# Kernel tuning notes

Hardware: AMD Instinct MI355X
Metric: run time of the kernel (lower is better)

The kernel has to match this reference:

```python
import jax, jax.numpy as jnp
import numpy as np

S = 10  # samples per node


def setup_inputs() -> dict:
    key = jax.random.key(0)
    k1, k2, k3, k4, k5, k6 = jax.random.split(key, 6)
    N, D, V, E, NNZ = 8192, 256, 32768, 100000, 262144
    z = jax.random.normal(k1, (N, D), dtype=jnp.float32)
    W = jax.random.normal(k2, (V, D), dtype=jnp.float32) * 0.02
    rand_u = jax.random.uniform(k3, (N, S), dtype=jnp.float32)
    edges = jax.random.randint(k4, (2, E), 0, N, dtype=jnp.int64)
    ptr = jnp.sort(jax.random.randint(k5, (N + 1,), 0, NNZ, dtype=jnp.int64))
    col = jax.random.randint(k6, (NNZ,), 0, N, dtype=jnp.int64)
    return {"z": z, "W": W, "rand_u": rand_u, "edges": edges, "ptr": ptr, "col": col}


def reference(z, W, rand_u, edges, ptr, col):
    N = z.shape[0]
    nnz = col.shape[0]
    deg = ptr[1:] - ptr[:-1]                                   # [N]
    # vectorized per-node uniform neighbor sampling (with replacement)
    samp = (rand_u * deg[:, None].astype(rand_u.dtype)).astype(jnp.int64)  # [N, S]
    gidx = jnp.clip(ptr[:-1, None] + samp, 0, nnz - 1)          # [N, S]
    self_idx = jnp.arange(N, dtype=col.dtype)[:, None]
    n_u = jnp.where(deg[:, None] > 0, col[gidx], self_idx)      # [N, S]
    # gather-sum aggregation, averaged with self
    u_aggr = (z[n_u].sum(axis=1) + z) / (S + 1)                 # [N, D]
    # predictor: Linear(no bias) + Softmax(dim=1)
    logits = jnp.einsum('nd,vd->nv', u_aggr, W)                 # [N, V]
    probs = jax.nn.softmax(logits, axis=1)
    h_u = probs[edges[0]]                                       # [E, V]
    # nn.CrossEntropyLoss applied to softmax outputs (faithful to original)
    tgt = edges[1]
    log_p = jax.nn.log_softmax(h_u, axis=1)
    loss = -log_p[jnp.arange(tgt.shape[0]), tgt].mean()
    return loss
```

## Files before the change

kernel.cpp:

```cpp
#include <hip/hip_runtime.h>
#include <hip/hip_bf16.h>
#include <stdint.h>


#define NODES 8192
#define DIM   256
#define VOCAB 32768
#define SAMP  10
#define LOG2E 1.4426950408889634f

typedef float  f32x4  __attribute__((ext_vector_type(4)));
typedef short  bf16x8 __attribute__((ext_vector_type(8)));
typedef unsigned short u16x4 __attribute__((ext_vector_type(4)));

static __device__ __forceinline__ unsigned short f2bf(float x) {
    __hip_bfloat16 b = __float2bfloat16(x);
    return *reinterpret_cast<unsigned short*>(&b);
}
static __device__ __forceinline__ float bf2f(unsigned short x) {
    union { unsigned int u; float f; } v; v.u = ((unsigned int)x) << 16; return v.f;
}
static __device__ __forceinline__ float fexp2(float x) {
    float r; asm("v_exp_f32 %0, %1" : "=v"(r) : "v"(x)); return r;
}

__global__ void k_aggregate(const float* __restrict__ z, const float* __restrict__ ru,
                            const int* __restrict__ ptr, const int* __restrict__ col,
                            unsigned short* __restrict__ ub, int nnz) {
    int wid = threadIdx.x >> 6, lane = threadIdx.x & 63;
    int node = blockIdx.x * 4 + wid;
    if (node >= NODES) return;
    int p0 = ptr[node], p1 = ptr[node + 1];
    int deg = p1 - p0;
    float fdeg = (float)deg;
    f32x4 acc = {0.f, 0.f, 0.f, 0.f};
    #pragma unroll
    for (int s = 0; s < SAMP; ++s) {
        float r = ru[node * SAMP + s];
        int samp = (int)(r * fdeg);
        int gidx = p0 + samp;
        gidx = gidx < 0 ? 0 : (gidx > nnz - 1 ? nnz - 1 : gidx);
        int nb = (deg > 0) ? col[gidx] : node;
        acc += ((const f32x4*)(z + (size_t)nb * DIM))[lane];
    }
    acc += ((const f32x4*)(z + (size_t)node * DIM))[lane];
    acc = acc * (LOG2E / 11.0f);
    u16x4 h;
    h.x = f2bf(acc.x); h.y = f2bf(acc.y); h.z = f2bf(acc.z); h.w = f2bf(acc.w);
    ((u16x4*)(ub + (size_t)node * DIM))[lane] = h;
}

__global__ void k_convert_w(const float* __restrict__ W, unsigned short* __restrict__ Wb, int n4) {
    int i = blockIdx.x * blockDim.x + threadIdx.x;
    if (i >= n4) return;
    f32x4 v = ((const f32x4*)W)[i];
    u16x4 h;
    h.x = f2bf(v.x); h.y = f2bf(v.y); h.z = f2bf(v.z); h.w = f2bf(v.w);
    ((u16x4*)Wb)[i] = h;
}

#define BM 128
#define BN 256
#define NSTEP 64

static __device__ __forceinline__ void gload_lds16(const void* g, void* l) {
    __builtin_amdgcn_global_load_lds(
        (const __attribute__((address_space(1))) unsigned int*)g,
        (__attribute__((address_space(3))) unsigned int*)l, 16, 0, 0);
}

__global__ __launch_bounds__(512)
__attribute__((amdgpu_waves_per_eu(2, 2)))
void k_gemm_stats(
        const unsigned short* __restrict__ A,
        const unsigned short* __restrict__ B,
        float* __restrict__ part_s) {
    __shared__ __align__(16) unsigned short Bs[4][BN * 64];
    __shared__ float sred[BM][4];

    const int bid = blockIdx.x;
    const int slab = bid & 7;
    const int ntile = bid >> 3;
    const int rm = ntile * BM;
    const int t = threadIdx.x;
    const int lane = t & 63;
    const int wid = t >> 6;
    const int wr = wid >> 2, wc = wid & 3;
    const int g = lane >> 4, r16 = lane & 15;

    const char* Bbase = (const char*)B + (size_t)slab * (4096u * 512u);
    const unsigned pre0 = ((unsigned)(t >> 3) << 9)
                        + ((unsigned)((t & 7) ^ ((t >> 3) & 7)) << 4);
    const unsigned ldsb = (unsigned)t << 4;

    auto stage = [&](int buf, int sigma) {
        unsigned soff = ((unsigned)(sigma >> 2) << 17) + ((unsigned)(sigma & 3) << 7);
        unsigned lb = (unsigned)buf * 32768u + ldsb;
        #pragma unroll
        for (int i = 0; i < 4; ++i)
            gload_lds16(Bbase + soff + pre0 + (unsigned)i * 32768u,
                        (char*)Bs + lb + (unsigned)i * 8192u);
    };

    bf16x8 areg[4][8];
    #pragma unroll
    for (int m = 0; m < 4; ++m)
        #pragma unroll
        for (int j = 0; j < 8; ++j)
            areg[m][j] = *(const bf16x8*)(A +
                (size_t)(rm + wr * 64 + m * 16 + r16) * DIM + (j * 4 + g) * 8);
    stage(0, 0);
    stage(1, 1);

    f32x4 acc[4][4] = {};
    f32x4 sv[4] = {};

    auto fold = [&]() {
        #pragma unroll
        for (int m = 0; m < 4; ++m)
            #pragma unroll
            for (int n = 0; n < 4; ++n) {
                #pragma unroll
                for (int r = 0; r < 4; ++r)
                    sv[m][r] += fexp2(acc[m][n][r]);
                acc[m][n] = (f32x4){0.f, 0.f, 0.f, 0.f};
            }
    };

    for (int c = 0; c < 16; ++c) {
        #pragma unroll
        for (int ks = 0; ks < 4; ++ks) {
            const int s = c * 4 + ks;
            asm volatile("s_waitcnt vmcnt(4)" ::: "memory");
            __builtin_amdgcn_s_barrier();
            { int sigma = s + 2; if (sigma >= NSTEP) sigma -= NSTEP;
              stage((s + 2) & 3, sigma); }
            if (ks == 0 && c > 0) fold();
            __builtin_amdgcn_s_setprio(1);
            #pragma unroll
            for (int kk = 0; kk < 2; ++kk) {
                bf16x8 bfr[4];
                #pragma unroll
                for (int n = 0; n < 4; ++n) {
                    int R = wc * 64 + n * 16 + r16;
                    int slot = (kk * 4 + g) ^ (R & 7);
                    bfr[n] = *(const bf16x8*)((const char*)Bs
                        + (unsigned)(s & 3) * 32768u + (unsigned)(R * 128 + slot * 16));
                }
                #pragma unroll
                for (int m = 0; m < 4; ++m)
                    #pragma unroll
                    for (int n = 0; n < 4; ++n)
                        acc[m][n] = __builtin_amdgcn_mfma_f32_16x16x32_bf16(
                            areg[m][ks * 2 + kk], bfr[n], acc[m][n], 0, 0, 0);
            }
            __builtin_amdgcn_s_setprio(0);
        }
    }
    fold();

    #pragma unroll
    for (int m = 0; m < 4; ++m)
        #pragma unroll
        for (int st = 1; st < 16; st <<= 1)
            #pragma unroll
            for (int r = 0; r < 4; ++r)
                sv[m][r] += __shfl_xor(sv[m][r], st, 64);
    if (r16 == 0)
        #pragma unroll
        for (int m = 0; m < 4; ++m)
            #pragma unroll
            for (int r = 0; r < 4; ++r)
                sred[wr * 64 + m * 16 + g * 4 + r][wc] = sv[m][r];
    __syncthreads();
    if (t < BM)
        part_s[(size_t)(rm + t) * 8 + slab] =
            sred[t][0] + sred[t][1] + sred[t][2] + sred[t][3];
}

__global__ void k_reduce(const float* __restrict__ part_s, float* __restrict__ s0) {
    int n = blockIdx.x * 256 + threadIdx.x;
    float s = 0.f;
    #pragma unroll
    for (int j = 0; j < 8; ++j) s += part_s[(size_t)n * 8 + j];
    s0[n] = s;
}

#define ELB 512
__global__ __launch_bounds__(256) void k_edge_loss(
        const unsigned short* __restrict__ ub, const unsigned short* __restrict__ Wb,
        const int* __restrict__ edges, const float* __restrict__ s0,
        float lse2c, float* __restrict__ partial, int E) {
    int wid = threadIdx.x >> 6, lane = threadIdx.x & 63;
    int w = blockIdx.x * 4 + wid;
    float local = 0.f;
    for (int e = w; e < E; e += ELB * 4) {
        int src = edges[e], tgt = edges[E + e];
        u16x4 a = ((const u16x4*)(ub + (size_t)src * DIM))[lane];
        u16x4 b = ((const u16x4*)(Wb + (size_t)tgt * DIM))[lane];
        float d = bf2f(a.x) * bf2f(b.x) + bf2f(a.y) * bf2f(b.y)
                + bf2f(a.z) * bf2f(b.z) + bf2f(a.w) * bf2f(b.w);
        #pragma unroll
        for (int st = 1; st < 64; st <<= 1) d += __shfl_xor(d, st, 64);
        if (lane == 0) local += lse2c - fexp2(d) / s0[src];
    }
    __shared__ float bs[4];
    if (lane == 0) bs[wid] = local;
    __syncthreads();
    if (threadIdx.x == 0) partial[blockIdx.x] = bs[0] + bs[1] + bs[2] + bs[3];
}

__global__ void k_final(const float* __restrict__ partial, float* __restrict__ out, float invE) {
    int t = threadIdx.x;
    float s = partial[t] + partial[t + 256];
    #pragma unroll
    for (int st = 1; st < 64; st <<= 1) s += __shfl_xor(s, st, 64);
    __shared__ float ls[4];
    if ((t & 63) == 0) ls[t >> 6] = s;
    __syncthreads();
    if (t == 0) out[0] = (ls[0] + ls[1] + ls[2] + ls[3]) * invE;
}

extern "C" void kernel_launch(void* const* d_in, const int* in_sizes, int n_in,
                              void* d_out, int out_size, void* d_ws, size_t ws_size,
                              hipStream_t stream) {
    const float* z    = (const float*)d_in[0];
    const float* W    = (const float*)d_in[1];
    const float* ru   = (const float*)d_in[2];
    const int* edges  = (const int*)d_in[3];
    const int* ptr    = (const int*)d_in[4];
    const int* col    = (const int*)d_in[5];
    const int E   = in_sizes[3] / 2;
    const int nnz = in_sizes[5];

    char* ws = (char*)d_ws;
    unsigned short* ub     = (unsigned short*)(ws + 0);
    unsigned short* Wb     = (unsigned short*)(ws + 4194304);
    float*          part_s = (float*)(ws + 20971520);
    float*          s0     = (float*)(ws + 21233664);
    float*          epart  = (float*)(ws + 21266432);
    float*          out    = (float*)d_out;

    const float lse2c = logf((float)VOCAB + 1.0f);

    hipLaunchKernelGGL(k_aggregate, dim3(NODES / 4), dim3(256), 0, stream, z, ru, ptr, col, ub, nnz);
    hipLaunchKernelGGL(k_convert_w, dim3(VOCAB * DIM / 4 / 256), dim3(256), 0, stream, W, Wb, VOCAB * DIM / 4);
    hipLaunchKernelGGL(k_gemm_stats, dim3(512), dim3(512), 0, stream, ub, Wb, part_s);
    hipLaunchKernelGGL(k_reduce, dim3(NODES / 256), dim3(256), 0, stream, part_s, s0);
    hipLaunchKernelGGL(k_edge_loss, dim3(ELB), dim3(256), 0, stream, ub, Wb, edges, s0, lse2c, epart, E);
    hipLaunchKernelGGL(k_final, dim3(1), dim3(256), 0, stream, epart, out, 1.0f / (float)E);
}
```

Measured before the change: 291.1 us.

## Double-step GEMM pipeline intervals, merge prep kernels, fold final reduction into atomics

The GEMM main loop now stages two K-steps per barrier interval with vmcnt(0), precomputes the LDS fragment offsets, and stops issuing the wrap-around redundant loads at the tail. Aggregation and the W-to-bf16 conversion run as one launch, and the final reduction kernel is replaced by per-block atomicAdd into the output, which k_reduce zeroes. The aim is fewer barriers and fewer launches. The trade-offs are coarser synchronisation that may expose load latency, and a non-deterministic float summation order.

```diff
diff --git a/kernel.cpp b/kernel.cpp
--- a/kernel.cpp
+++ b/kernel.cpp
@@ -24,39 +24,40 @@
     float r; asm("v_exp_f32 %0, %1" : "=v"(r) : "v"(x)); return r;
 }
 
-__global__ void k_aggregate(const float* __restrict__ z, const float* __restrict__ ru,
-                            const int* __restrict__ ptr, const int* __restrict__ col,
-                            unsigned short* __restrict__ ub, int nnz) {
-    int wid = threadIdx.x >> 6, lane = threadIdx.x & 63;
-    int node = blockIdx.x * 4 + wid;
-    if (node >= NODES) return;
-    int p0 = ptr[node], p1 = ptr[node + 1];
-    int deg = p1 - p0;
-    float fdeg = (float)deg;
-    f32x4 acc = {0.f, 0.f, 0.f, 0.f};
-    #pragma unroll
-    for (int s = 0; s < SAMP; ++s) {
-        float r = ru[node * SAMP + s];
-        int samp = (int)(r * fdeg);
-        int gidx = p0 + samp;
-        gidx = gidx < 0 ? 0 : (gidx > nnz - 1 ? nnz - 1 : gidx);
-        int nb = (deg > 0) ? col[gidx] : node;
-        acc += ((const f32x4*)(z + (size_t)nb * DIM))[lane];
+__global__ void k_agg_conv(const float* __restrict__ z, const float* __restrict__ ru,
+                           const int* __restrict__ ptr, const int* __restrict__ col,
+                           const float* __restrict__ W,
+                           unsigned short* __restrict__ ub, unsigned short* __restrict__ Wb,
+                           int nnz) {
+    int b = blockIdx.x;
+    if (b < 2048) {
+        int wid = threadIdx.x >> 6, lane = threadIdx.x & 63;
+        int node = b * 4 + wid;
+        int p0 = ptr[node], p1 = ptr[node + 1];
+        int deg = p1 - p0;
+        float fdeg = (float)deg;
+        f32x4 acc = {0.f, 0.f, 0.f, 0.f};
+        #pragma unroll
+        for (int s = 0; s < SAMP; ++s) {
+            float r = ru[node * SAMP + s];
+            int samp = (int)(r * fdeg);
+            int gidx = p0 + samp;
+            gidx = gidx < 0 ? 0 : (gidx > nnz - 1 ? nnz - 1 : gidx);
+            int nb = (deg > 0) ? col[gidx] : node;
+            acc += ((const f32x4*)(z + (size_t)nb * DIM))[lane];
+        }
+        acc += ((const f32x4*)(z + (size_t)node * DIM))[lane];
+        acc = acc * (LOG2E / 11.0f);
+        u16x4 h;
+        h.x = f2bf(acc.x); h.y = f2bf(acc.y); h.z = f2bf(acc.z); h.w = f2bf(acc.w);
+        ((u16x4*)(ub + (size_t)node * DIM))[lane] = h;
+    } else {
+        int i = (b - 2048) * 256 + threadIdx.x;
+        f32x4 v = ((const f32x4*)W)[i];
+        u16x4 h;
+        h.x = f2bf(v.x); h.y = f2bf(v.y); h.z = f2bf(v.z); h.w = f2bf(v.w);
+        ((u16x4*)Wb)[i] = h;
     }
-    acc += ((const f32x4*)(z + (size_t)node * DIM))[lane];
-    acc = acc * (LOG2E / 11.0f);
-    u16x4 h;
-    h.x = f2bf(acc.x); h.y = f2bf(acc.y); h.z = f2bf(acc.z); h.w = f2bf(acc.w);
-    ((u16x4*)(ub + (size_t)node * DIM))[lane] = h;
-}
-
-__global__ void k_convert_w(const float* __restrict__ W, unsigned short* __restrict__ Wb, int n4) {
-    int i = blockIdx.x * blockDim.x + threadIdx.x;
-    if (i >= n4) return;
-    f32x4 v = ((const f32x4*)W)[i];
-    u16x4 h;
-    h.x = f2bf(v.x); h.y = f2bf(v.y); h.z = f2bf(v.z); h.w = f2bf(v.w);
-    ((u16x4*)Wb)[i] = h;
 }
 
 #define BM 128
@@ -93,15 +94,25 @@
                         + ((unsigned)((t & 7) ^ ((t >> 3) & 7)) << 4);
     const unsigned ldsb = (unsigned)t << 4;
 
-    auto stage = [&](int buf, int sigma) {
+    auto stage = [&](int sigma) {
         unsigned soff = ((unsigned)(sigma >> 2) << 17) + ((unsigned)(sigma & 3) << 7);
-        unsigned lb = (unsigned)buf * 32768u + ldsb;
+        unsigned lb = (unsigned)(sigma & 3) * 32768u + ldsb;
         #pragma unroll
         for (int i = 0; i < 4; ++i)
             gload_lds16(Bbase + soff + pre0 + (unsigned)i * 32768u,
                         (char*)Bs + lb + (unsigned)i * 8192u);
     };
 
+    unsigned boffs[8];
+    #pragma unroll
+    for (int kk = 0; kk < 2; ++kk)
+        #pragma unroll
+        for (int n = 0; n < 4; ++n) {
+            int R = wc * 64 + n * 16 + r16;
+            int slot = (kk * 4 + g) ^ (R & 7);
+            boffs[kk * 4 + n] = (unsigned)(R * 128 + slot * 16);
+        }
+
     bf16x8 areg[4][8];
     #pragma unroll
     for (int m = 0; m < 4; ++m)
@@ -109,8 +120,8 @@
         for (int j = 0; j < 8; ++j)
             areg[m][j] = *(const bf16x8*)(A +
                 (size_t)(rm + wr * 64 + m * 16 + r16) * DIM + (j * 4 + g) * 8);
-    stage(0, 0);
-    stage(1, 1);
+    stage(0);
+    stage(1);
 
     f32x4 acc[4][4] = {};
     f32x4 sv[4] = {};
@@ -127,37 +138,41 @@
             }
     };
 
+#define STEP(KS, TT) do {                                                     \
+    const unsigned lb_ = (unsigned)((TT) & 3) * 32768u;                       \
+    bf16x8 bfr[8];                                                            \
+    _Pragma("unroll")                                                         \
+    for (int q = 0; q < 8; ++q)                                               \
+        bfr[q] = *(const bf16x8*)((const char*)Bs + lb_ + boffs[q]);          \
+    __builtin_amdgcn_s_setprio(1);                                            \
+    _Pragma("unroll")                                                         \
+    for (int kk = 0; kk < 2; ++kk)                                            \
+        _Pragma("unroll")                                                     \
+        for (int m = 0; m < 4; ++m)                                           \
+            _Pragma("unroll")                                                 \
+            for (int n = 0; n < 4; ++n)                                       \
+                acc[m][n] = __builtin_amdgcn_mfma_f32_16x16x32_bf16(          \
+                    areg[m][(KS) * 2 + kk], bfr[kk * 4 + n], acc[m][n], 0, 0, 0); \
+    __builtin_amdgcn_s_setprio(0);                                            \
+} while (0)
+
+#define INTERVAL(TB, KSA, KSB, DOFOLD) do {                                   \
+    asm volatile("s_waitcnt vmcnt(0)" ::: "memory");                          \
+    __builtin_amdgcn_s_barrier();                                             \
+    __builtin_amdgcn_sched_barrier(0);                                        \
+    if ((TB) + 2 < NSTEP) stage((TB) + 2);                                    \
+    if ((TB) + 3 < NSTEP) stage((TB) + 3);                                    \
+    STEP(KSA, TB);                                                            \
+    STEP(KSB, (TB) + 1);                                                      \
+    if (DOFOLD) fold();                                                       \
+} while (0)
+
     for (int c = 0; c < 16; ++c) {
-        #pragma unroll
-        for (int ks = 0; ks < 4; ++ks) {
-            const int s = c * 4 + ks;
-            asm volatile("s_waitcnt vmcnt(4)" ::: "memory");
-            __builtin_amdgcn_s_barrier();
-            { int sigma = s + 2; if (sigma >= NSTEP) sigma -= NSTEP;
-              stage((s + 2) & 3, sigma); }
-            if (ks == 0 && c > 0) fold();
-            __builtin_amdgcn_s_setprio(1);
-            #pragma unroll
-            for (int kk = 0; kk < 2; ++kk) {
-                bf16x8 bfr[4];
-                #pragma unroll
-                for (int n = 0; n < 4; ++n) {
-                    int R = wc * 64 + n * 16 + r16;
-                    int slot = (kk * 4 + g) ^ (R & 7);
-                    bfr[n] = *(const bf16x8*)((const char*)Bs
-                        + (unsigned)(s & 3) * 32768u + (unsigned)(R * 128 + slot * 16));
-                }
-                #pragma unroll
-                for (int m = 0; m < 4; ++m)
-                    #pragma unroll
-                    for (int n = 0; n < 4; ++n)
-                        acc[m][n] = __builtin_amdgcn_mfma_f32_16x16x32_bf16(
-                            areg[m][ks * 2 + kk], bfr[n], acc[m][n], 0, 0, 0);
-            }
-            __builtin_amdgcn_s_setprio(0);
-        }
+        INTERVAL(c * 4 + 0, 0, 1, 0);
+        INTERVAL(c * 4 + 2, 2, 3, 1);
     }
-    fold();
+#undef INTERVAL
+#undef STEP
 
     #pragma unroll
     for (int m = 0; m < 4; ++m)
@@ -178,19 +193,21 @@
             sred[t][0] + sred[t][1] + sred[t][2] + sred[t][3];
 }
 
-__global__ void k_reduce(const float* __restrict__ part_s, float* __restrict__ s0) {
+__global__ void k_reduce(const float* __restrict__ part_s, float* __restrict__ s0,
+                         float* __restrict__ out) {
     int n = blockIdx.x * 256 + threadIdx.x;
     float s = 0.f;
     #pragma unroll
     for (int j = 0; j < 8; ++j) s += part_s[(size_t)n * 8 + j];
     s0[n] = s;
+    if (n == 0) out[0] = 0.f;
 }
 
 #define ELB 512
 __global__ __launch_bounds__(256) void k_edge_loss(
         const unsigned short* __restrict__ ub, const unsigned short* __restrict__ Wb,
         const int* __restrict__ edges, const float* __restrict__ s0,
-        float lse2c, float* __restrict__ partial, int E) {
+        float lse2c, float* __restrict__ out, int E, float invE) {
     int wid = threadIdx.x >> 6, lane = threadIdx.x & 63;
     int w = blockIdx.x * 4 + wid;
     float local = 0.f;
@@ -207,18 +224,8 @@
     __shared__ float bs[4];
     if (lane == 0) bs[wid] = local;
     __syncthreads();
-    if (threadIdx.x == 0) partial[blockIdx.x] = bs[0] + bs[1] + bs[2] + bs[3];
-}
-
-__global__ void k_final(const float* __restrict__ partial, float* __restrict__ out, float invE) {
-    int t = threadIdx.x;
-    float s = partial[t] + partial[t + 256];
-    #pragma unroll
-    for (int st = 1; st < 64; st <<= 1) s += __shfl_xor(s, st, 64);
-    __shared__ float ls[4];
-    if ((t & 63) == 0) ls[t >> 6] = s;
-    __syncthreads();
-    if (t == 0) out[0] = (ls[0] + ls[1] + ls[2] + ls[3]) * invE;
+    if (threadIdx.x == 0)
+        atomicAdd(out, (bs[0] + bs[1] + bs[2] + bs[3]) * invE);
 }
 
 extern "C" void kernel_launch(void* const* d_in, const int* in_sizes, int n_in,
@@ -238,15 +245,14 @@
     unsigned short* Wb     = (unsigned short*)(ws + 4194304);
     float*          part_s = (float*)(ws + 20971520);
     float*          s0     = (float*)(ws + 21233664);
-    float*          epart  = (float*)(ws + 21266432);
     float*          out    = (float*)d_out;
 
     const float lse2c = logf((float)VOCAB + 1.0f);
 
-    hipLaunchKernelGGL(k_aggregate, dim3(NODES / 4), dim3(256), 0, stream, z, ru, ptr, col, ub, nnz);
-    hipLaunchKernelGGL(k_convert_w, dim3(VOCAB * DIM / 4 / 256), dim3(256), 0, stream, W, Wb, VOCAB * DIM / 4);
+    hipLaunchKernelGGL(k_agg_conv, dim3(2048 + VOCAB * DIM / 4 / 256), dim3(256), 0, stream,
+                       z, ru, ptr, col, W, ub, Wb, nnz);
     hipLaunchKernelGGL(k_gemm_stats, dim3(512), dim3(512), 0, stream, ub, Wb, part_s);
-    hipLaunchKernelGGL(k_reduce, dim3(NODES / 256), dim3(256), 0, stream, part_s, s0);
-    hipLaunchKernelGGL(k_edge_loss, dim3(ELB), dim3(256), 0, stream, ub, Wb, edges, s0, lse2c, epart, E);
-    hipLaunchKernelGGL(k_final, dim3(1), dim3(256), 0, stream, epart, out, 1.0f / (float)E);
-}
+    hipLaunchKernelGGL(k_reduce, dim3(NODES / 256), dim3(256), 0, stream, part_s, s0, out);
+    hipLaunchKernelGGL(k_edge_loss, dim3(ELB), dim3(256), 0, stream, ub, Wb, edges, s0,
+                       lse2c, out, E, 1.0f / (float)E);
+}
```

Result: no change. 290.4 us (-0.2%).
